# Kernel optimization log

Measured on AMD Instinct MI355X. Metric: run time of the kernel, lower is better.

Reference implementation:

```python
import jax, jax.numpy as jnp
import numpy as np

WS = 8            # window size (square)
NUM_HEADS = 8
DIM = 256
IMG = 256         # feature map H=W for mask construction
SHIFT = WS // 2
B = 4


def _rel_pos_index(Wh, Ww):
    coords = np.stack(np.meshgrid(np.arange(Wh), np.arange(Ww), indexing='ij'))  # (2,Wh,Ww)
    cf = coords.reshape(2, -1)
    rel = cf[:, :, None] - cf[:, None, :]        # (2,N,N)
    rel = rel.transpose(1, 2, 0).astype(np.int64)
    rel[..., 0] += Wh - 1
    rel[..., 1] += Ww - 1
    rel[..., 0] *= 2 * Ww - 1
    return rel.sum(-1)                           # (N,N)


def _shift_mask(H, W, ws, ss):
    # standard Swin shifted-window attention mask: (nW, ws*ws, ws*ws) with 0 / -100
    img = np.zeros((H, W), dtype=np.float32)
    cnt = 0
    for hs in (slice(0, -ws), slice(-ws, -ss), slice(-ss, None)):
        for wsl in (slice(0, -ws), slice(-ws, -ss), slice(-ss, None)):
            img[hs, wsl] = cnt
            cnt += 1
    m = img.reshape(H // ws, ws, W // ws, ws).transpose(0, 2, 1, 3).reshape(-1, ws * ws)
    am = m[:, None, :] - m[:, :, None]
    return np.where(am != 0, np.float32(-100.0), np.float32(0.0))


def setup_inputs() -> dict:
    key = jax.random.key(0)
    ks = jax.random.split(key, 10)
    nW = (IMG // WS) ** 2
    B_ = B * nW
    N = WS * WS
    x = jax.random.normal(ks[0], (B_, N, DIM), dtype=jnp.float32)
    y = jax.random.normal(ks[1], (B_, N, DIM), dtype=jnp.float32)
    mask = jnp.asarray(_shift_mask(IMG, IMG, WS, SHIFT))
    s = 0.02
    q_w = jax.random.normal(ks[2], (DIM, DIM), dtype=jnp.float32) * s
    q_b = jnp.zeros((DIM,), dtype=jnp.float32)
    kv_w = jax.random.normal(ks[3], (2 * DIM, DIM), dtype=jnp.float32) * s
    kv_b = jnp.zeros((2 * DIM,), dtype=jnp.float32)
    proj_w = jax.random.normal(ks[4], (DIM, DIM), dtype=jnp.float32) * s
    proj_b = jnp.zeros((DIM,), dtype=jnp.float32)
    rpb_table = jax.random.normal(ks[5], ((2 * WS - 1) ** 2, NUM_HEADS), dtype=jnp.float32) * s
    return {"x": x, "y": y, "mask": mask, "q_w": q_w, "q_b": q_b,
            "kv_w": kv_w, "kv_b": kv_b, "proj_w": proj_w, "proj_b": proj_b,
            "rpb_table": rpb_table}


def reference(x, y, mask, q_w, q_b, kv_w, kv_b, proj_w, proj_b, rpb_table):
    B_, N, C = x.shape
    H = NUM_HEADS
    hd = C // H
    scale = hd ** -0.5
    # projections
    q = (x @ q_w.T + q_b).reshape(B_, N, H, hd).transpose(0, 2, 1, 3) * scale  # (B_,H,N,hd)
    kv = (y @ kv_w.T + kv_b).reshape(B_, N, 2, H, hd)
    k = kv[:, :, 0].transpose(0, 2, 1, 3)  # (B_,H,N,hd)
    v = kv[:, :, 1].transpose(0, 2, 1, 3)
    attn = jnp.einsum('bhid,bhjd->bhij', q, k)  # (B_,H,N,N)
    # relative position bias gathered from table
    rpi = jnp.asarray(_rel_pos_index(WS, WS))           # (N,N) int
    bias = rpb_table[rpi.reshape(-1)].reshape(N, N, H).transpose(2, 0, 1)  # (H,N,N)
    attn = attn + bias[None]
    # shifted-window mask
    nW = mask.shape[0]
    attn = attn.reshape(B_ // nW, nW, H, N, N) + mask[None, :, None]
    attn = attn.reshape(B_, H, N, N)
    attn = jax.nn.softmax(attn, axis=-1)
    out = jnp.einsum('bhij,bhjd->bhid', attn, v)        # (B_,H,N,hd)
    out = out.transpose(0, 2, 1, 3).reshape(B_, N, C)
    return out @ proj_w.T + proj_b
```

## Files before the change

kernel.cpp:

```cpp
#include <hip/hip_runtime.h>

typedef _Float16 half_t;
typedef _Float16 half8  __attribute__((ext_vector_type(8)));
typedef _Float16 half4v __attribute__((ext_vector_type(4)));
typedef float    f32x4  __attribute__((ext_vector_type(4)));

#define ROWB   528
#define S_A    0
#define S_B    33792
#define SMEM_BYTES 67584
#define SCALE  0.17677669529663687f

__global__ __launch_bounds__(256) void swin_prep(
    const float* __restrict__ q_w, const float* __restrict__ kv_w,
    const float* __restrict__ proj_w, const float* __restrict__ rpb,
    const float* __restrict__ mask,
    half_t* __restrict__ w16, half_t* __restrict__ fused)
{
    int t = blockIdx.x * 256 + threadIdx.x;
    if (t < 65536)        w16[t] = (half_t)(q_w[t] * SCALE);
    else if (t < 196608)  w16[t] = (half_t)kv_w[t - 65536];
    else if (t < 262144)  w16[t] = (half_t)proj_w[t - 196608];
    else if (t < 393216) {
        int u = t - 262144;
        int cls = u >> 15, rest = u & 32767;
        int h = rest >> 12, i = (rest >> 6) & 63, j = rest & 63;
        int idx = ((i >> 3) - (j >> 3) + 7) * 15 + ((i & 7) - (j & 7) + 7);
        int wsel = (cls == 0) ? 0 : (cls == 1) ? 31 : (cls == 2) ? 992 : 1023;
        fused[u] = (half_t)(rpb[idx * 8 + h] + mask[(size_t)wsel * 4096 + i * 64 + j]);
    }
}

static __device__ __forceinline__ unsigned pk2(float a, float b) {
    union { _Float16 h[2]; unsigned u; } t;
    t.h[0] = (_Float16)a; t.h[1] = (_Float16)b; return t.u;
}

#define BUILD_FRAG(dst, P0, P1)                                          \
    do {                                                                 \
        union { unsigned u[4]; half8 h; } _u;                            \
        _Pragma("unroll")                                                \
        for (int p = 0; p < 4; ++p) {                                    \
            int _src = (p >> 1) ? srcB : srcA;                           \
            unsigned _rlo = (unsigned)__shfl((int)(P0)[p & 1], _src);    \
            unsigned _rhi = (unsigned)__shfl((int)(P1)[p & 1], _src);    \
            _u.u[p] = hi ? _rhi : _rlo;                                  \
        }                                                                \
        dst = _u.h;                                                      \
    } while (0)

__global__ __launch_bounds__(512, 2) void swin_main(
    const float* __restrict__ x, const float* __restrict__ y,
    const float* __restrict__ q_b, const float* __restrict__ kv_b,
    const float* __restrict__ proj_b,
    const half_t* __restrict__ w16, const half_t* __restrict__ fused,
    float* __restrict__ out)
{
    __shared__ __align__(16) char sm[SMEM_BYTES];
    const int tid  = threadIdx.x;
    const int w    = tid >> 6;
    const int lane = tid & 63;
    const int l15  = lane & 15;
    const int g    = lane >> 4;
    const int b    = blockIdx.x;
    const int jf0  = w * 32;
    const int srcA = ((2 * g) & 3) * 16 + l15;
    const int srcB = ((2 * g + 1) & 3) * 16 + l15;
    const int hi   = g >> 1;

    const float* xb = x + (size_t)b * 16384;
    const float* yb = y + (size_t)b * 16384;
    const half_t* wkv = w16 + 65536;

    {
        float4 fx[8], fy[8];
        #pragma unroll
        for (int it = 0; it < 4; ++it) {
            int c = tid + it * 512;
            int row = c >> 5, c8 = c & 31;
            fx[it*2+0] = *(const float4*)(xb + row * 256 + c8 * 8);
            fx[it*2+1] = *(const float4*)(xb + row * 256 + c8 * 8 + 4);
            fy[it*2+0] = *(const float4*)(yb + row * 256 + c8 * 8);
            fy[it*2+1] = *(const float4*)(yb + row * 256 + c8 * 8 + 4);
        }
        #pragma unroll
        for (int it = 0; it < 4; ++it) {
            int c = tid + it * 512;
            int row = c >> 5, c8 = c & 31;
            half8 hx, hy;
            #pragma unroll
            for (int e = 0; e < 4; ++e) {
                hx[e]   = (half_t)(&fx[it*2+0].x)[e];
                hx[e+4] = (half_t)(&fx[it*2+1].x)[e];
                hy[e]   = (half_t)(&fy[it*2+0].x)[e];
                hy[e+4] = (half_t)(&fy[it*2+1].x)[e];
            }
            int off = row * ROWB + c8 * 16;
            *(half8*)(sm + S_A + off) = hx;
            *(half8*)(sm + S_B + off) = hy;
        }
    }
    __syncthreads();

    f32x4 kacc[2][4], vacc[4][2];
    #pragma unroll
    for (int ft = 0; ft < 2; ++ft)
        #pragma unroll
        for (int tok = 0; tok < 4; ++tok) {
            f32x4 z = {0.f,0.f,0.f,0.f}; kacc[ft][tok] = z; vacc[tok][ft] = z;
        }
    #pragma unroll
    for (int kh = 0; kh < 4; ++kh) {
        half8 wbk[2][2], wbv[2][2];
        #pragma unroll
        for (int k2 = 0; k2 < 2; ++k2) {
            int k0 = (kh * 2 + k2) * 32 + g * 8;
            #pragma unroll
            for (int ft = 0; ft < 2; ++ft) {
                int jf = jf0 + ft * 16 + l15;
                wbk[k2][ft] = *(const half8*)(wkv + jf * 256 + k0);
                wbv[k2][ft] = *(const half8*)(wkv + (256 + jf) * 256 + k0);
            }
        }
        #pragma unroll
        for (int k2 = 0; k2 < 2; ++k2) {
            int k0 = (kh * 2 + k2) * 32 + g * 8;
            half8 a[4];
            #pragma unroll
            for (int tok = 0; tok < 4; ++tok)
                a[tok] = *(const half8*)(sm + S_B + (tok * 16 + l15) * ROWB + k0 * 2);
            #pragma unroll
            for (int ft = 0; ft < 2; ++ft)
                #pragma unroll
                for (int tok = 0; tok < 4; ++tok) {
                    kacc[ft][tok] = __builtin_amdgcn_mfma_f32_16x16x32_f16(wbk[k2][ft], a[tok], kacc[ft][tok], 0, 0, 0);
                    vacc[tok][ft] = __builtin_amdgcn_mfma_f32_16x16x32_f16(a[tok], wbv[k2][ft], vacc[tok][ft], 0, 0, 0);
                }
        }
    }

    unsigned kp[2][4][2], vp[4][2][2];
    #pragma unroll
    for (int ft = 0; ft < 2; ++ft) {
        float4 kb4 = *(const float4*)(kv_b + jf0 + ft * 16 + g * 4);
        #pragma unroll
        for (int tok = 0; tok < 4; ++tok) {
            kp[ft][tok][0] = pk2(kacc[ft][tok][0] + kb4.x, kacc[ft][tok][1] + kb4.y);
            kp[ft][tok][1] = pk2(kacc[ft][tok][2] + kb4.z, kacc[ft][tok][3] + kb4.w);
        }
    }
    #pragma unroll
    for (int ft = 0; ft < 2; ++ft) {
        float vb = kv_b[256 + jf0 + ft * 16 + l15];
        #pragma unroll
        for (int tok = 0; tok < 4; ++tok) {
            vp[tok][ft][0] = pk2(vacc[tok][ft][0] + vb, vacc[tok][ft][1] + vb);
            vp[tok][ft][1] = pk2(vacc[tok][ft][2] + vb, vacc[tok][ft][3] + vb);
        }
    }

    unsigned qp[2][4][2];
    {
        f32x4 qacc[2][4];
        #pragma unroll
        for (int ft = 0; ft < 2; ++ft)
            #pragma unroll
            for (int tok = 0; tok < 4; ++tok) { f32x4 z = {0.f,0.f,0.f,0.f}; qacc[ft][tok] = z; }
        #pragma unroll
        for (int kh = 0; kh < 4; ++kh) {
            half8 wbq[2][2];
            #pragma unroll
            for (int k2 = 0; k2 < 2; ++k2) {
                int k0 = (kh * 2 + k2) * 32 + g * 8;
                #pragma unroll
                for (int ft = 0; ft < 2; ++ft)
                    wbq[k2][ft] = *(const half8*)(w16 + (jf0 + ft * 16 + l15) * 256 + k0);
            }
            #pragma unroll
            for (int k2 = 0; k2 < 2; ++k2) {
                int k0 = (kh * 2 + k2) * 32 + g * 8;
                half8 a[4];
                #pragma unroll
                for (int tok = 0; tok < 4; ++tok)
                    a[tok] = *(const half8*)(sm + S_A + (tok * 16 + l15) * ROWB + k0 * 2);
                #pragma unroll
                for (int ft = 0; ft < 2; ++ft)
                    #pragma unroll
                    for (int tok = 0; tok < 4; ++tok)
                        qacc[ft][tok] = __builtin_amdgcn_mfma_f32_16x16x32_f16(wbq[k2][ft], a[tok], qacc[ft][tok], 0, 0, 0);
            }
        }
        #pragma unroll
        for (int ft = 0; ft < 2; ++ft) {
            float4 qb4 = *(const float4*)(q_b + jf0 + ft * 16 + g * 4);
            #pragma unroll
            for (int tok = 0; tok < 4; ++tok) {
                qp[ft][tok][0] = pk2(qacc[ft][tok][0] + qb4.x * SCALE, qacc[ft][tok][1] + qb4.y * SCALE);
                qp[ft][tok][1] = pk2(qacc[ft][tok][2] + qb4.z * SCALE, qacc[ft][tok][3] + qb4.w * SCALE);
            }
        }
    }

    f32x4 o[2][4];
    {
        half8 ka[4], qf[4];
        #pragma unroll
        for (int mt = 0; mt < 4; ++mt) BUILD_FRAG(ka[mt], kp[0][mt], kp[1][mt]);
        #pragma unroll
        for (int nt = 0; nt < 4; ++nt) BUILD_FRAG(qf[nt], qp[0][nt], qp[1][nt]);

        f32x4 t[4][4];
        #pragma unroll
        for (int mt = 0; mt < 4; ++mt)
            #pragma unroll
            for (int nt = 0; nt < 4; ++nt) {
                f32x4 z = {0.f,0.f,0.f,0.f};
                t[mt][nt] = __builtin_amdgcn_mfma_f32_16x16x32_f16(ka[mt], qf[nt], z, 0, 0, 0);
            }

        const int wi = b & 1023;
        const int cls = ((((wi >> 5) == 31) ? 2 : 0)) | (((wi & 31) == 31) ? 1 : 0);
        const half_t* fb = fused + ((size_t)cls * 8 + w) * 4096;
        half4v fm[4][4];
        #pragma unroll
        for (int nt = 0; nt < 4; ++nt)
            #pragma unroll
            for (int mt = 0; mt < 4; ++mt)
                fm[nt][mt] = *(const half4v*)(fb + (nt * 16 + l15) * 64 + mt * 16 + g * 4);

        #pragma unroll
        for (int nt = 0; nt < 4; ++nt) {
            #pragma unroll
            for (int mt = 0; mt < 4; ++mt)
                #pragma unroll
                for (int r = 0; r < 4; ++r)
                    t[mt][nt][r] += (float)fm[nt][mt][r];
            float m = -1e30f;
            #pragma unroll
            for (int mt = 0; mt < 4; ++mt)
                #pragma unroll
                for (int r = 0; r < 4; ++r) m = fmaxf(m, t[mt][nt][r]);
            m = fmaxf(m, __shfl_xor(m, 16));
            m = fmaxf(m, __shfl_xor(m, 32));
            float s = 0.f;
            #pragma unroll
            for (int mt = 0; mt < 4; ++mt)
                #pragma unroll
                for (int r = 0; r < 4; ++r) {
                    float p = __expf(t[mt][nt][r] - m);
                    t[mt][nt][r] = p;
                    s += p;
                }
            s += __shfl_xor(s, 16);
            s += __shfl_xor(s, 32);
            float inv = 1.f / s;
            #pragma unroll
            for (int mt = 0; mt < 4; ++mt)
                #pragma unroll
                for (int r = 0; r < 4; ++r) t[mt][nt][r] *= inv;
        }

        unsigned pp[4][4][2];
        #pragma unroll
        for (int mt = 0; mt < 4; ++mt)
            #pragma unroll
            for (int nt = 0; nt < 4; ++nt) {
                pp[mt][nt][0] = pk2(t[mt][nt][0], t[mt][nt][1]);
                pp[mt][nt][1] = pk2(t[mt][nt][2], t[mt][nt][3]);
            }

        #pragma unroll
        for (int dt = 0; dt < 2; ++dt)
            #pragma unroll
            for (int nt = 0; nt < 4; ++nt) { f32x4 z = {0.f,0.f,0.f,0.f}; o[dt][nt] = z; }
        #pragma unroll
        for (int kc = 0; kc < 2; ++kc) {
            half8 va[2], pf[4];
            #pragma unroll
            for (int dt = 0; dt < 2; ++dt) BUILD_FRAG(va[dt], vp[kc*2+0][dt], vp[kc*2+1][dt]);
            #pragma unroll
            for (int nt = 0; nt < 4; ++nt) BUILD_FRAG(pf[nt], pp[kc*2+0][nt], pp[kc*2+1][nt]);
            #pragma unroll
            for (int dt = 0; dt < 2; ++dt)
                #pragma unroll
                for (int nt = 0; nt < 4; ++nt)
                    o[dt][nt] = __builtin_amdgcn_mfma_f32_16x16x32_f16(va[dt], pf[nt], o[dt][nt], 0, 0, 0);
        }
    }

    __syncthreads();

    #pragma unroll
    for (int nt = 0; nt < 4; ++nt) {
        int i = nt * 16 + l15;
        #pragma unroll
        for (int dt = 0; dt < 2; ++dt) {
            half4v ov;
            ov[0] = (half_t)o[dt][nt][0];
            ov[1] = (half_t)o[dt][nt][1];
            ov[2] = (half_t)o[dt][nt][2];
            ov[3] = (half_t)o[dt][nt][3];
            *(half4v*)(sm + S_B + i * ROWB + (jf0 + dt * 16 + g * 4) * 2) = ov;
        }
    }
    __syncthreads();

    {
        const half_t* wp = w16 + 196608;
        f32x4 dacc[4][2];
        #pragma unroll
        for (int mt = 0; mt < 4; ++mt)
            #pragma unroll
            for (int ft = 0; ft < 2; ++ft) { f32x4 z = {0.f,0.f,0.f,0.f}; dacc[mt][ft] = z; }
        #pragma unroll
        for (int kh = 0; kh < 4; ++kh) {
            half8 wbp[2][2];
            #pragma unroll
            for (int k2 = 0; k2 < 2; ++k2) {
                int k0 = (kh * 2 + k2) * 32 + g * 8;
                #pragma unroll
                for (int ft = 0; ft < 2; ++ft)
                    wbp[k2][ft] = *(const half8*)(wp + (jf0 + ft * 16 + l15) * 256 + k0);
            }
            #pragma unroll
            for (int k2 = 0; k2 < 2; ++k2) {
                int k0 = (kh * 2 + k2) * 32 + g * 8;
                half8 a[4];
                #pragma unroll
                for (int mt = 0; mt < 4; ++mt)
                    a[mt] = *(const half8*)(sm + S_B + (mt * 16 + l15) * ROWB + k0 * 2);
                #pragma unroll
                for (int mt = 0; mt < 4; ++mt)
                    #pragma unroll
                    for (int ft = 0; ft < 2; ++ft)
                        dacc[mt][ft] = __builtin_amdgcn_mfma_f32_16x16x32_f16(wbp[k2][ft], a[mt], dacc[mt][ft], 0, 0, 0);
            }
        }
        float* ob = out + (size_t)b * 16384;
        #pragma unroll
        for (int ft = 0; ft < 2; ++ft) {
            float4 pb4 = *(const float4*)(proj_b + jf0 + ft * 16 + g * 4);
            #pragma unroll
            for (int mt = 0; mt < 4; ++mt) {
                float4 v;
                v.x = dacc[mt][ft][0] + pb4.x;
                v.y = dacc[mt][ft][1] + pb4.y;
                v.z = dacc[mt][ft][2] + pb4.z;
                v.w = dacc[mt][ft][3] + pb4.w;
                *(float4*)(ob + (mt * 16 + l15) * 256 + jf0 + ft * 16 + g * 4) = v;
            }
        }
    }
}

extern "C" void kernel_launch(void* const* d_in, const int* in_sizes, int n_in,
                              void* d_out, int out_size, void* d_ws, size_t ws_size,
                              hipStream_t stream) {
    const float* x      = (const float*)d_in[0];
    const float* y      = (const float*)d_in[1];
    const float* mask   = (const float*)d_in[2];
    const float* q_w    = (const float*)d_in[3];
    const float* q_b    = (const float*)d_in[4];
    const float* kv_w   = (const float*)d_in[5];
    const float* kv_b   = (const float*)d_in[6];
    const float* proj_w = (const float*)d_in[7];
    const float* proj_b = (const float*)d_in[8];
    const float* rpb    = (const float*)d_in[9];

    half_t* w16   = (half_t*)d_ws;
    half_t* fused = (half_t*)((char*)d_ws + 524288);

    swin_prep<<<1536, 256, 0, stream>>>(q_w, kv_w, proj_w, rpb, mask, w16, fused);
    swin_main<<<4096, 512, 0, stream>>>(x, y, q_b, kv_b, proj_b,
                                        w16, fused, (float*)d_out);
}
```

Measured before the change: 469.4 us.

## Make main kernel persistent over 8 windows per block with setprio and nontemporal stores

Each block now loops over 8 windows instead of one, and the grid shrinks from 4096 to 512 blocks. Bias vectors are hoisted out of the loop, MFMA sections are wrapped in s_setprio, and output stores become nontemporal. Barriers are replaced with a custom lgkmcnt wait plus s_barrier so the next window's global loads can be issued before the barrier. The goal is to amortize block launch and bias loads. The risk is fewer blocks (512 over 256 CUs at 2 per CU) with less latency hiding, plus a serial tail.

```diff
diff --git a/kernel.cpp b/kernel.cpp
--- a/kernel.cpp
+++ b/kernel.cpp
@@ -10,6 +10,13 @@
 #define S_B    33792
 #define SMEM_BYTES 67584
 #define SCALE  0.17677669529663687f
+#define NWPB   8
+
+#define BAR() do { \
+    asm volatile("s_waitcnt lgkmcnt(0)" ::: "memory"); \
+    __builtin_amdgcn_s_barrier(); \
+    __builtin_amdgcn_sched_barrier(0); \
+} while (0)
 
 __global__ __launch_bounds__(256) void swin_prep(
     const float* __restrict__ q_w, const float* __restrict__ kv_w,
@@ -62,17 +69,31 @@
     const int lane = tid & 63;
     const int l15  = lane & 15;
     const int g    = lane >> 4;
-    const int b    = blockIdx.x;
     const int jf0  = w * 32;
     const int srcA = ((2 * g) & 3) * 16 + l15;
     const int srcB = ((2 * g + 1) & 3) * 16 + l15;
     const int hi   = g >> 1;
-
-    const float* xb = x + (size_t)b * 16384;
-    const float* yb = y + (size_t)b * 16384;
     const half_t* wkv = w16 + 65536;
-
-    {
+    const half_t* wpj = w16 + 196608;
+
+    float4 kb4[2], qb4s[2], pb4[2];
+    float  vb[2];
+    #pragma unroll
+    for (int ft = 0; ft < 2; ++ft) {
+        kb4[ft]  = *(const float4*)(kv_b + jf0 + ft * 16 + g * 4);
+        float4 q4 = *(const float4*)(q_b + jf0 + ft * 16 + g * 4);
+        qb4s[ft].x = q4.x * SCALE; qb4s[ft].y = q4.y * SCALE;
+        qb4s[ft].z = q4.z * SCALE; qb4s[ft].w = q4.w * SCALE;
+        pb4[ft]  = *(const float4*)(proj_b + jf0 + ft * 16 + g * 4);
+        vb[ft]   = kv_b[256 + jf0 + ft * 16 + l15];
+    }
+
+    #pragma unroll 1
+    for (int wd = 0; wd < NWPB; ++wd) {
+        const int b = blockIdx.x * NWPB + wd;
+        const float* xb = x + (size_t)b * 16384;
+        const float* yb = y + (size_t)b * 16384;
+
         float4 fx[8], fy[8];
         #pragma unroll
         for (int it = 0; it < 4; ++it) {
@@ -83,6 +104,9 @@
             fy[it*2+0] = *(const float4*)(yb + row * 256 + c8 * 8);
             fy[it*2+1] = *(const float4*)(yb + row * 256 + c8 * 8 + 4);
         }
+
+        BAR();
+
         #pragma unroll
         for (int it = 0; it < 4; ++it) {
             int c = tid + it * 512;
@@ -99,82 +123,28 @@
             *(half8*)(sm + S_A + off) = hx;
             *(half8*)(sm + S_B + off) = hy;
         }
-    }
-    __syncthreads();
-
-    f32x4 kacc[2][4], vacc[4][2];
-    #pragma unroll
-    for (int ft = 0; ft < 2; ++ft)
-        #pragma unroll
-        for (int tok = 0; tok < 4; ++tok) {
-            f32x4 z = {0.f,0.f,0.f,0.f}; kacc[ft][tok] = z; vacc[tok][ft] = z;
-        }
-    #pragma unroll
-    for (int kh = 0; kh < 4; ++kh) {
-        half8 wbk[2][2], wbv[2][2];
-        #pragma unroll
-        for (int k2 = 0; k2 < 2; ++k2) {
-            int k0 = (kh * 2 + k2) * 32 + g * 8;
-            #pragma unroll
-            for (int ft = 0; ft < 2; ++ft) {
-                int jf = jf0 + ft * 16 + l15;
-                wbk[k2][ft] = *(const half8*)(wkv + jf * 256 + k0);
-                wbv[k2][ft] = *(const half8*)(wkv + (256 + jf) * 256 + k0);
-            }
-        }
-        #pragma unroll
-        for (int k2 = 0; k2 < 2; ++k2) {
-            int k0 = (kh * 2 + k2) * 32 + g * 8;
-            half8 a[4];
-            #pragma unroll
-            for (int tok = 0; tok < 4; ++tok)
-                a[tok] = *(const half8*)(sm + S_B + (tok * 16 + l15) * ROWB + k0 * 2);
-            #pragma unroll
-            for (int ft = 0; ft < 2; ++ft)
-                #pragma unroll
-                for (int tok = 0; tok < 4; ++tok) {
-                    kacc[ft][tok] = __builtin_amdgcn_mfma_f32_16x16x32_f16(wbk[k2][ft], a[tok], kacc[ft][tok], 0, 0, 0);
-                    vacc[tok][ft] = __builtin_amdgcn_mfma_f32_16x16x32_f16(a[tok], wbv[k2][ft], vacc[tok][ft], 0, 0, 0);
-                }
-        }
-    }
-
-    unsigned kp[2][4][2], vp[4][2][2];
-    #pragma unroll
-    for (int ft = 0; ft < 2; ++ft) {
-        float4 kb4 = *(const float4*)(kv_b + jf0 + ft * 16 + g * 4);
-        #pragma unroll
-        for (int tok = 0; tok < 4; ++tok) {
-            kp[ft][tok][0] = pk2(kacc[ft][tok][0] + kb4.x, kacc[ft][tok][1] + kb4.y);
-            kp[ft][tok][1] = pk2(kacc[ft][tok][2] + kb4.z, kacc[ft][tok][3] + kb4.w);
-        }
-    }
-    #pragma unroll
-    for (int ft = 0; ft < 2; ++ft) {
-        float vb = kv_b[256 + jf0 + ft * 16 + l15];
-        #pragma unroll
-        for (int tok = 0; tok < 4; ++tok) {
-            vp[tok][ft][0] = pk2(vacc[tok][ft][0] + vb, vacc[tok][ft][1] + vb);
-            vp[tok][ft][1] = pk2(vacc[tok][ft][2] + vb, vacc[tok][ft][3] + vb);
-        }
-    }
-
-    unsigned qp[2][4][2];
-    {
-        f32x4 qacc[2][4];
+
+        BAR();
+
+        f32x4 kacc[2][4], vacc[4][2];
         #pragma unroll
         for (int ft = 0; ft < 2; ++ft)
             #pragma unroll
-            for (int tok = 0; tok < 4; ++tok) { f32x4 z = {0.f,0.f,0.f,0.f}; qacc[ft][tok] = z; }
+            for (int tok = 0; tok < 4; ++tok) {
+                f32x4 z = {0.f,0.f,0.f,0.f}; kacc[ft][tok] = z; vacc[tok][ft] = z;
+            }
         #pragma unroll
         for (int kh = 0; kh < 4; ++kh) {
-            half8 wbq[2][2];
+            half8 wbk[2][2], wbv[2][2];
             #pragma unroll
             for (int k2 = 0; k2 < 2; ++k2) {
                 int k0 = (kh * 2 + k2) * 32 + g * 8;
                 #pragma unroll
-                for (int ft = 0; ft < 2; ++ft)
-                    wbq[k2][ft] = *(const half8*)(w16 + (jf0 + ft * 16 + l15) * 256 + k0);
+                for (int ft = 0; ft < 2; ++ft) {
+                    int jf = jf0 + ft * 16 + l15;
+                    wbk[k2][ft] = *(const half8*)(wkv + jf * 256 + k0);
+                    wbv[k2][ft] = *(const half8*)(wkv + (256 + jf) * 256 + k0);
+                }
             }
             #pragma unroll
             for (int k2 = 0; k2 < 2; ++k2) {
@@ -182,172 +152,225 @@
                 half8 a[4];
                 #pragma unroll
                 for (int tok = 0; tok < 4; ++tok)
-                    a[tok] = *(const half8*)(sm + S_A + (tok * 16 + l15) * ROWB + k0 * 2);
+                    a[tok] = *(const half8*)(sm + S_B + (tok * 16 + l15) * ROWB + k0 * 2);
+                __builtin_amdgcn_s_setprio(1);
                 #pragma unroll
                 for (int ft = 0; ft < 2; ++ft)
                     #pragma unroll
+                    for (int tok = 0; tok < 4; ++tok) {
+                        kacc[ft][tok] = __builtin_amdgcn_mfma_f32_16x16x32_f16(wbk[k2][ft], a[tok], kacc[ft][tok], 0, 0, 0);
+                        vacc[tok][ft] = __builtin_amdgcn_mfma_f32_16x16x32_f16(a[tok], wbv[k2][ft], vacc[tok][ft], 0, 0, 0);
+                    }
+                __builtin_amdgcn_s_setprio(0);
+            }
+        }
+
+        unsigned kp[2][4][2], vp[4][2][2];
+        #pragma unroll
+        for (int ft = 0; ft < 2; ++ft)
+            #pragma unroll
+            for (int tok = 0; tok < 4; ++tok) {
+                kp[ft][tok][0] = pk2(kacc[ft][tok][0] + kb4[ft].x, kacc[ft][tok][1] + kb4[ft].y);
+                kp[ft][tok][1] = pk2(kacc[ft][tok][2] + kb4[ft].z, kacc[ft][tok][3] + kb4[ft].w);
+                vp[tok][ft][0] = pk2(vacc[tok][ft][0] + vb[ft], vacc[tok][ft][1] + vb[ft]);
+                vp[tok][ft][1] = pk2(vacc[tok][ft][2] + vb[ft], vacc[tok][ft][3] + vb[ft]);
+            }
+
+        unsigned qp[2][4][2];
+        {
+            f32x4 qacc[2][4];
+            #pragma unroll
+            for (int ft = 0; ft < 2; ++ft)
+                #pragma unroll
+                for (int tok = 0; tok < 4; ++tok) { f32x4 z = {0.f,0.f,0.f,0.f}; qacc[ft][tok] = z; }
+            #pragma unroll
+            for (int kh = 0; kh < 4; ++kh) {
+                half8 wbq[2][2];
+                #pragma unroll
+                for (int k2 = 0; k2 < 2; ++k2) {
+                    int k0 = (kh * 2 + k2) * 32 + g * 8;
+                    #pragma unroll
+                    for (int ft = 0; ft < 2; ++ft)
+                        wbq[k2][ft] = *(const half8*)(w16 + (jf0 + ft * 16 + l15) * 256 + k0);
+                }
+                #pragma unroll
+                for (int k2 = 0; k2 < 2; ++k2) {
+                    int k0 = (kh * 2 + k2) * 32 + g * 8;
+                    half8 a[4];
+                    #pragma unroll
                     for (int tok = 0; tok < 4; ++tok)
-                        qacc[ft][tok] = __builtin_amdgcn_mfma_f32_16x16x32_f16(wbq[k2][ft], a[tok], qacc[ft][tok], 0, 0, 0);
-            }
-        }
-        #pragma unroll
-        for (int ft = 0; ft < 2; ++ft) {
-            float4 qb4 = *(const float4*)(q_b + jf0 + ft * 16 + g * 4);
-            #pragma unroll
-            for (int tok = 0; tok < 4; ++tok) {
-                qp[ft][tok][0] = pk2(qacc[ft][tok][0] + qb4.x * SCALE, qacc[ft][tok][1] + qb4.y * SCALE);
-                qp[ft][tok][1] = pk2(qacc[ft][tok][2] + qb4.z * SCALE, qacc[ft][tok][3] + qb4.w * SCALE);
-            }
-        }
-    }
-
-    f32x4 o[2][4];
-    {
-        half8 ka[4], qf[4];
-        #pragma unroll
-        for (int mt = 0; mt < 4; ++mt) BUILD_FRAG(ka[mt], kp[0][mt], kp[1][mt]);
-        #pragma unroll
-        for (int nt = 0; nt < 4; ++nt) BUILD_FRAG(qf[nt], qp[0][nt], qp[1][nt]);
-
-        f32x4 t[4][4];
-        #pragma unroll
-        for (int mt = 0; mt < 4; ++mt)
+                        a[tok] = *(const half8*)(sm + S_A + (tok * 16 + l15) * ROWB + k0 * 2);
+                    __builtin_amdgcn_s_setprio(1);
+                    #pragma unroll
+                    for (int ft = 0; ft < 2; ++ft)
+                        #pragma unroll
+                        for (int tok = 0; tok < 4; ++tok)
+                            qacc[ft][tok] = __builtin_amdgcn_mfma_f32_16x16x32_f16(wbq[k2][ft], a[tok], qacc[ft][tok], 0, 0, 0);
+                    __builtin_amdgcn_s_setprio(0);
+                }
+            }
+            #pragma unroll
+            for (int ft = 0; ft < 2; ++ft)
+                #pragma unroll
+                for (int tok = 0; tok < 4; ++tok) {
+                    qp[ft][tok][0] = pk2(qacc[ft][tok][0] + qb4s[ft].x, qacc[ft][tok][1] + qb4s[ft].y);
+                    qp[ft][tok][1] = pk2(qacc[ft][tok][2] + qb4s[ft].z, qacc[ft][tok][3] + qb4s[ft].w);
+                }
+        }
+
+        f32x4 o[2][4];
+        {
+            half8 ka[4], qf[4];
+            #pragma unroll
+            for (int mt = 0; mt < 4; ++mt) BUILD_FRAG(ka[mt], kp[0][mt], kp[1][mt]);
+            #pragma unroll
+            for (int nt = 0; nt < 4; ++nt) BUILD_FRAG(qf[nt], qp[0][nt], qp[1][nt]);
+
+            f32x4 t[4][4];
+            __builtin_amdgcn_s_setprio(1);
+            #pragma unroll
+            for (int mt = 0; mt < 4; ++mt)
+                #pragma unroll
+                for (int nt = 0; nt < 4; ++nt) {
+                    f32x4 z = {0.f,0.f,0.f,0.f};
+                    t[mt][nt] = __builtin_amdgcn_mfma_f32_16x16x32_f16(ka[mt], qf[nt], z, 0, 0, 0);
+                }
+            __builtin_amdgcn_s_setprio(0);
+
+            const int wi = b & 1023;
+            const int cls = ((((wi >> 5) == 31) ? 2 : 0)) | (((wi & 31) == 31) ? 1 : 0);
+            const half_t* fb = fused + ((size_t)cls * 8 + w) * 4096;
+            half4v fm[4][4];
+            #pragma unroll
+            for (int nt = 0; nt < 4; ++nt)
+                #pragma unroll
+                for (int mt = 0; mt < 4; ++mt)
+                    fm[nt][mt] = *(const half4v*)(fb + (nt * 16 + l15) * 64 + mt * 16 + g * 4);
+
             #pragma unroll
             for (int nt = 0; nt < 4; ++nt) {
-                f32x4 z = {0.f,0.f,0.f,0.f};
-                t[mt][nt] = __builtin_amdgcn_mfma_f32_16x16x32_f16(ka[mt], qf[nt], z, 0, 0, 0);
-            }
-
-        const int wi = b & 1023;
-        const int cls = ((((wi >> 5) == 31) ? 2 : 0)) | (((wi & 31) == 31) ? 1 : 0);
-        const half_t* fb = fused + ((size_t)cls * 8 + w) * 4096;
-        half4v fm[4][4];
-        #pragma unroll
-        for (int nt = 0; nt < 4; ++nt)
+                #pragma unroll
+                for (int mt = 0; mt < 4; ++mt)
+                    #pragma unroll
+                    for (int r = 0; r < 4; ++r)
+                        t[mt][nt][r] += (float)fm[nt][mt][r];
+                float m = -1e30f;
+                #pragma unroll
+                for (int mt = 0; mt < 4; ++mt)
+                    #pragma unroll
+                    for (int r = 0; r < 4; ++r) m = fmaxf(m, t[mt][nt][r]);
+                m = fmaxf(m, __shfl_xor(m, 16));
+                m = fmaxf(m, __shfl_xor(m, 32));
+                float s = 0.f;
+                #pragma unroll
+                for (int mt = 0; mt < 4; ++mt)
+                    #pragma unroll
+                    for (int r = 0; r < 4; ++r) {
+                        float p = __expf(t[mt][nt][r] - m);
+                        t[mt][nt][r] = p;
+                        s += p;
+                    }
+                s += __shfl_xor(s, 16);
+                s += __shfl_xor(s, 32);
+                float inv = 1.f / s;
+                #pragma unroll
+                for (int mt = 0; mt < 4; ++mt)
+                    #pragma unroll
+                    for (int r = 0; r < 4; ++r) t[mt][nt][r] *= inv;
+            }
+
+            unsigned pp[4][4][2];
             #pragma unroll
             for (int mt = 0; mt < 4; ++mt)
-                fm[nt][mt] = *(const half4v*)(fb + (nt * 16 + l15) * 64 + mt * 16 + g * 4);
+                #pragma unroll
+                for (int nt = 0; nt < 4; ++nt) {
+                    pp[mt][nt][0] = pk2(t[mt][nt][0], t[mt][nt][1]);
+                    pp[mt][nt][1] = pk2(t[mt][nt][2], t[mt][nt][3]);
+                }
+
+            #pragma unroll
+            for (int dt = 0; dt < 2; ++dt)
+                #pragma unroll
+                for (int nt = 0; nt < 4; ++nt) { f32x4 z = {0.f,0.f,0.f,0.f}; o[dt][nt] = z; }
+            #pragma unroll
+            for (int kc = 0; kc < 2; ++kc) {
+                half8 va[2], pf[4];
+                #pragma unroll
+                for (int dt = 0; dt < 2; ++dt) BUILD_FRAG(va[dt], vp[kc*2+0][dt], vp[kc*2+1][dt]);
+                #pragma unroll
+                for (int nt = 0; nt < 4; ++nt) BUILD_FRAG(pf[nt], pp[kc*2+0][nt], pp[kc*2+1][nt]);
+                __builtin_amdgcn_s_setprio(1);
+                #pragma unroll
+                for (int dt = 0; dt < 2; ++dt)
+                    #pragma unroll
+                    for (int nt = 0; nt < 4; ++nt)
+                        o[dt][nt] = __builtin_amdgcn_mfma_f32_16x16x32_f16(va[dt], pf[nt], o[dt][nt], 0, 0, 0);
+                __builtin_amdgcn_s_setprio(0);
+            }
+        }
+
+        BAR();
 
         #pragma unroll
         for (int nt = 0; nt < 4; ++nt) {
+            int i = nt * 16 + l15;
+            #pragma unroll
+            for (int dt = 0; dt < 2; ++dt) {
+                half4v ov;
+                ov[0] = (half_t)o[dt][nt][0];
+                ov[1] = (half_t)o[dt][nt][1];
+                ov[2] = (half_t)o[dt][nt][2];
+                ov[3] = (half_t)o[dt][nt][3];
+                *(half4v*)(sm + S_B + i * ROWB + (jf0 + dt * 16 + g * 4) * 2) = ov;
+            }
+        }
+
+        BAR();
+
+        {
+            f32x4 dacc[4][2];
             #pragma unroll
             for (int mt = 0; mt < 4; ++mt)
                 #pragma unroll
-                for (int r = 0; r < 4; ++r)
-                    t[mt][nt][r] += (float)fm[nt][mt][r];
-            float m = -1e30f;
-            #pragma unroll
-            for (int mt = 0; mt < 4; ++mt)
-                #pragma unroll
-                for (int r = 0; r < 4; ++r) m = fmaxf(m, t[mt][nt][r]);
-            m = fmaxf(m, __shfl_xor(m, 16));
-            m = fmaxf(m, __shfl_xor(m, 32));
-            float s = 0.f;
-            #pragma unroll
-            for (int mt = 0; mt < 4; ++mt)
-                #pragma unroll
-                for (int r = 0; r < 4; ++r) {
-                    float p = __expf(t[mt][nt][r] - m);
-                    t[mt][nt][r] = p;
-                    s += p;
-                }
-            s += __shfl_xor(s, 16);
-            s += __shfl_xor(s, 32);
-            float inv = 1.f / s;
-            #pragma unroll
-            for (int mt = 0; mt < 4; ++mt)
-                #pragma unroll
-                for (int r = 0; r < 4; ++r) t[mt][nt][r] *= inv;
-        }
-
-        unsigned pp[4][4][2];
-        #pragma unroll
-        for (int mt = 0; mt < 4; ++mt)
-            #pragma unroll
-            for (int nt = 0; nt < 4; ++nt) {
-                pp[mt][nt][0] = pk2(t[mt][nt][0], t[mt][nt][1]);
-                pp[mt][nt][1] = pk2(t[mt][nt][2], t[mt][nt][3]);
-            }
-
-        #pragma unroll
-        for (int dt = 0; dt < 2; ++dt)
-            #pragma unroll
-            for (int nt = 0; nt < 4; ++nt) { f32x4 z = {0.f,0.f,0.f,0.f}; o[dt][nt] = z; }
-        #pragma unroll
-        for (int kc = 0; kc < 2; ++kc) {
-            half8 va[2], pf[4];
-            #pragma unroll
-            for (int dt = 0; dt < 2; ++dt) BUILD_FRAG(va[dt], vp[kc*2+0][dt], vp[kc*2+1][dt]);
-            #pragma unroll
-            for (int nt = 0; nt < 4; ++nt) BUILD_FRAG(pf[nt], pp[kc*2+0][nt], pp[kc*2+1][nt]);
-            #pragma unroll
-            for (int dt = 0; dt < 2; ++dt)
-                #pragma unroll
-                for (int nt = 0; nt < 4; ++nt)
-                    o[dt][nt] = __builtin_amdgcn_mfma_f32_16x16x32_f16(va[dt], pf[nt], o[dt][nt], 0, 0, 0);
-        }
-    }
-
-    __syncthreads();
-
-    #pragma unroll
-    for (int nt = 0; nt < 4; ++nt) {
-        int i = nt * 16 + l15;
-        #pragma unroll
-        for (int dt = 0; dt < 2; ++dt) {
-            half4v ov;
-            ov[0] = (half_t)o[dt][nt][0];
-            ov[1] = (half_t)o[dt][nt][1];
-            ov[2] = (half_t)o[dt][nt][2];
-            ov[3] = (half_t)o[dt][nt][3];
-            *(half4v*)(sm + S_B + i * ROWB + (jf0 + dt * 16 + g * 4) * 2) = ov;
-        }
-    }
-    __syncthreads();
-
-    {
-        const half_t* wp = w16 + 196608;
-        f32x4 dacc[4][2];
-        #pragma unroll
-        for (int mt = 0; mt < 4; ++mt)
-            #pragma unroll
-            for (int ft = 0; ft < 2; ++ft) { f32x4 z = {0.f,0.f,0.f,0.f}; dacc[mt][ft] = z; }
-        #pragma unroll
-        for (int kh = 0; kh < 4; ++kh) {
-            half8 wbp[2][2];
-            #pragma unroll
-            for (int k2 = 0; k2 < 2; ++k2) {
-                int k0 = (kh * 2 + k2) * 32 + g * 8;
-                #pragma unroll
-                for (int ft = 0; ft < 2; ++ft)
-                    wbp[k2][ft] = *(const half8*)(wp + (jf0 + ft * 16 + l15) * 256 + k0);
-            }
-            #pragma unroll
-            for (int k2 = 0; k2 < 2; ++k2) {
-                int k0 = (kh * 2 + k2) * 32 + g * 8;
-                half8 a[4];
-                #pragma unroll
-                for (int mt = 0; mt < 4; ++mt)
-                    a[mt] = *(const half8*)(sm + S_B + (mt * 16 + l15) * ROWB + k0 * 2);
-                #pragma unroll
-                for (int mt = 0; mt < 4; ++mt)
+                for (int ft = 0; ft < 2; ++ft) { f32x4 z = {0.f,0.f,0.f,0.f}; dacc[mt][ft] = z; }
+            #pragma unroll
+            for (int kh = 0; kh < 4; ++kh) {
+                half8 wbp[2][2];
+                #pragma unroll
+                for (int k2 = 0; k2 < 2; ++k2) {
+                    int k0 = (kh * 2 + k2) * 32 + g * 8;
                     #pragma unroll
                     for (int ft = 0; ft < 2; ++ft)
-                        dacc[mt][ft] = __builtin_amdgcn_mfma_f32_16x16x32_f16(wbp[k2][ft], a[mt], dacc[mt][ft], 0, 0, 0);
-            }
-        }
-        float* ob = out + (size_t)b * 16384;
-        #pragma unroll
-        for (int ft = 0; ft < 2; ++ft) {
-            float4 pb4 = *(const float4*)(proj_b + jf0 + ft * 16 + g * 4);
-            #pragma unroll
-            for (int mt = 0; mt < 4; ++mt) {
-                float4 v;
-                v.x = dacc[mt][ft][0] + pb4.x;
-                v.y = dacc[mt][ft][1] + pb4.y;
-                v.z = dacc[mt][ft][2] + pb4.z;
-                v.w = dacc[mt][ft][3] + pb4.w;
-                *(float4*)(ob + (mt * 16 + l15) * 256 + jf0 + ft * 16 + g * 4) = v;
+                        wbp[k2][ft] = *(const half8*)(wpj + (jf0 + ft * 16 + l15) * 256 + k0);
+                }
+                #pragma unroll
+                for (int k2 = 0; k2 < 2; ++k2) {
+                    int k0 = (kh * 2 + k2) * 32 + g * 8;
+                    half8 a[4];
+                    #pragma unroll
+                    for (int mt = 0; mt < 4; ++mt)
+                        a[mt] = *(const half8*)(sm + S_B + (mt * 16 + l15) * ROWB + k0 * 2);
+                    __builtin_amdgcn_s_setprio(1);
+                    #pragma unroll
+                    for (int mt = 0; mt < 4; ++mt)
+                        #pragma unroll
+                        for (int ft = 0; ft < 2; ++ft)
+                            dacc[mt][ft] = __builtin_amdgcn_mfma_f32_16x16x32_f16(wbp[k2][ft], a[mt], dacc[mt][ft], 0, 0, 0);
+                    __builtin_amdgcn_s_setprio(0);
+                }
+            }
+            float* ob = out + (size_t)b * 16384;
+            #pragma unroll
+            for (int ft = 0; ft < 2; ++ft) {
+                #pragma unroll
+                for (int mt = 0; mt < 4; ++mt) {
+                    f32x4 v;
+                    v[0] = dacc[mt][ft][0] + pb4[ft].x;
+                    v[1] = dacc[mt][ft][1] + pb4[ft].y;
+                    v[2] = dacc[mt][ft][2] + pb4[ft].z;
+                    v[3] = dacc[mt][ft][3] + pb4[ft].w;
+                    __builtin_nontemporal_store(v, (f32x4*)(ob + (mt * 16 + l15) * 256 + jf0 + ft * 16 + g * 4));
+                }
             }
         }
     }
@@ -361,8 +384,8 @@
     const float* mask   = (const float*)d_in[2];
     const float* q_w    = (const float*)d_in[3];
     const float* q_b    = (const float*)d_in[4];
+    const float* kv_b   = (const float*)d_in[6];
     const float* kv_w   = (const float*)d_in[5];
-    const float* kv_b   = (const float*)d_in[6];
     const float* proj_w = (const float*)d_in[7];
     const float* proj_b = (const float*)d_in[8];
     const float* rpb    = (const float*)d_in[9];
@@ -371,6 +394,6 @@
     half_t* fused = (half_t*)((char*)d_ws + 524288);
 
     swin_prep<<<1536, 256, 0, stream>>>(q_w, kv_w, proj_w, rpb, mask, w16, fused);
-    swin_main<<<4096, 512, 0, stream>>>(x, y, q_b, kv_b, proj_b,
-                                        w16, fused, (float*)d_out);
+    swin_main<<<512, 512, 0, stream>>>(x, y, q_b, kv_b, proj_b,
+                                       w16, fused, (float*)d_out);
 }
```

Measured after the change: 486.1 us. 3.6% more time.

## Split fused Swin window attention into QKV, attention and projection kernels

Applied to the files above, without the earlier changes.

Breaks the single fused kernel into three kernels (QKV projection, attention, output projection) that exchange Q, K, transposed V and O through global workspace in fp16, chunked by available workspace size. The aim is to remove register pressure and cross-lane shuffles in the fused kernel and allow different occupancy per stage. In exchange it adds a large global-memory round trip per window and extra kernel launches.

```diff
diff --git a/kernel.cpp b/kernel.cpp
--- a/kernel.cpp
+++ b/kernel.cpp
@@ -8,7 +8,8 @@
 #define ROWB   528
 #define S_A    0
 #define S_B    33792
-#define SMEM_BYTES 67584
+#define K1_SMEM 67584
+#define K3_SMEM 33792
 #define SCALE  0.17677669529663687f
 
 __global__ __launch_bounds__(256) void swin_prep(
@@ -35,6 +36,9 @@
     union { _Float16 h[2]; unsigned u; } t;
     t.h[0] = (_Float16)a; t.h[1] = (_Float16)b; return t.u;
 }
+static __device__ __forceinline__ half4v h4(float a, float b, float c, float d) {
+    half4v v; v[0] = (half_t)a; v[1] = (half_t)b; v[2] = (half_t)c; v[3] = (half_t)d; return v;
+}
 
 #define BUILD_FRAG(dst, P0, P1)                                          \
     do {                                                                 \
@@ -49,28 +53,26 @@
         dst = _u.h;                                                      \
     } while (0)
 
-__global__ __launch_bounds__(512, 2) void swin_main(
+__global__ __launch_bounds__(512, 1) void swin_qkv(
     const float* __restrict__ x, const float* __restrict__ y,
     const float* __restrict__ q_b, const float* __restrict__ kv_b,
-    const float* __restrict__ proj_b,
-    const half_t* __restrict__ w16, const half_t* __restrict__ fused,
-    float* __restrict__ out)
+    const half_t* __restrict__ w16,
+    half_t* __restrict__ Qg, half_t* __restrict__ Kg, half_t* __restrict__ Vtg,
+    int b0)
 {
-    __shared__ __align__(16) char sm[SMEM_BYTES];
+    __shared__ __align__(16) char sm[K1_SMEM];
     const int tid  = threadIdx.x;
     const int w    = tid >> 6;
     const int lane = tid & 63;
     const int l15  = lane & 15;
     const int g    = lane >> 4;
-    const int b    = blockIdx.x;
+    const int bl   = blockIdx.x;
+    const int b    = b0 + bl;
     const int jf0  = w * 32;
-    const int srcA = ((2 * g) & 3) * 16 + l15;
-    const int srcB = ((2 * g + 1) & 3) * 16 + l15;
-    const int hi   = g >> 1;
+    const half_t* wkv = w16 + 65536;
 
     const float* xb = x + (size_t)b * 16384;
     const float* yb = y + (size_t)b * 16384;
-    const half_t* wkv = w16 + 65536;
 
     {
         float4 fx[8], fy[8];
@@ -138,28 +140,29 @@
                 }
         }
     }
-
-    unsigned kp[2][4][2], vp[4][2][2];
-    #pragma unroll
-    for (int ft = 0; ft < 2; ++ft) {
-        float4 kb4 = *(const float4*)(kv_b + jf0 + ft * 16 + g * 4);
-        #pragma unroll
-        for (int tok = 0; tok < 4; ++tok) {
-            kp[ft][tok][0] = pk2(kacc[ft][tok][0] + kb4.x, kacc[ft][tok][1] + kb4.y);
-            kp[ft][tok][1] = pk2(kacc[ft][tok][2] + kb4.z, kacc[ft][tok][3] + kb4.w);
-        }
-    }
-    #pragma unroll
-    for (int ft = 0; ft < 2; ++ft) {
-        float vb = kv_b[256 + jf0 + ft * 16 + l15];
-        #pragma unroll
-        for (int tok = 0; tok < 4; ++tok) {
-            vp[tok][ft][0] = pk2(vacc[tok][ft][0] + vb, vacc[tok][ft][1] + vb);
-            vp[tok][ft][1] = pk2(vacc[tok][ft][2] + vb, vacc[tok][ft][3] + vb);
-        }
-    }
-
-    unsigned qp[2][4][2];
+    {
+        half_t* Kw = Kg + (size_t)bl * 16384;
+        #pragma unroll
+        for (int ft = 0; ft < 2; ++ft) {
+            float4 kb4 = *(const float4*)(kv_b + jf0 + ft * 16 + g * 4);
+            #pragma unroll
+            for (int tok = 0; tok < 4; ++tok)
+                *(half4v*)(Kw + (tok * 16 + l15) * 256 + jf0 + ft * 16 + g * 4) =
+                    h4(kacc[ft][tok][0] + kb4.x, kacc[ft][tok][1] + kb4.y,
+                       kacc[ft][tok][2] + kb4.z, kacc[ft][tok][3] + kb4.w);
+        }
+        half_t* Vw = Vtg + (size_t)bl * 16384;
+        #pragma unroll
+        for (int ft = 0; ft < 2; ++ft) {
+            float vb = kv_b[256 + jf0 + ft * 16 + l15];
+            #pragma unroll
+            for (int tok = 0; tok < 4; ++tok)
+                *(half4v*)(Vw + (jf0 + ft * 16 + l15) * 64 + tok * 16 + g * 4) =
+                    h4(vacc[tok][ft][0] + vb, vacc[tok][ft][1] + vb,
+                       vacc[tok][ft][2] + vb, vacc[tok][ft][3] + vb);
+    }
+    }
+
     {
         f32x4 qacc[2][4];
         #pragma unroll
@@ -190,165 +193,202 @@
                         qacc[ft][tok] = __builtin_amdgcn_mfma_f32_16x16x32_f16(wbq[k2][ft], a[tok], qacc[ft][tok], 0, 0, 0);
             }
         }
+        half_t* Qw = Qg + (size_t)bl * 16384;
         #pragma unroll
         for (int ft = 0; ft < 2; ++ft) {
-            float4 qb4 = *(const float4*)(q_b + jf0 + ft * 16 + g * 4);
-            #pragma unroll
-            for (int tok = 0; tok < 4; ++tok) {
-                qp[ft][tok][0] = pk2(qacc[ft][tok][0] + qb4.x * SCALE, qacc[ft][tok][1] + qb4.y * SCALE);
-                qp[ft][tok][1] = pk2(qacc[ft][tok][2] + qb4.z * SCALE, qacc[ft][tok][3] + qb4.w * SCALE);
+            float4 q4 = *(const float4*)(q_b + jf0 + ft * 16 + g * 4);
+            #pragma unroll
+            for (int tok = 0; tok < 4; ++tok)
+                *(half4v*)(Qw + (tok * 16 + l15) * 256 + jf0 + ft * 16 + g * 4) =
+                    h4(qacc[ft][tok][0] + q4.x * SCALE, qacc[ft][tok][1] + q4.y * SCALE,
+                       qacc[ft][tok][2] + q4.z * SCALE, qacc[ft][tok][3] + q4.w * SCALE);
+        }
+    }
+}
+
+__global__ __launch_bounds__(512, 1) void swin_attn(
+    const half_t* __restrict__ Qg, const half_t* __restrict__ Kg,
+    const half_t* __restrict__ Vtg, const half_t* __restrict__ fused,
+    half_t* __restrict__ Og, int b0)
+{
+    const int tid  = threadIdx.x;
+    const int w    = tid >> 6;
+    const int lane = tid & 63;
+    const int l15  = lane & 15;
+    const int g    = lane >> 4;
+    const int bl   = blockIdx.x;
+    const int b    = b0 + bl;
+    const int jf0  = w * 32;
+    const int srcA = ((2 * g) & 3) * 16 + l15;
+    const int srcB = ((2 * g + 1) & 3) * 16 + l15;
+    const int hi   = g >> 1;
+
+    const half_t* Qw = Qg + (size_t)bl * 16384;
+    const half_t* Kw = Kg + (size_t)bl * 16384;
+    const half_t* Vw = Vtg + (size_t)bl * 16384;
+
+    half8 ka[4], qf[4];
+    #pragma unroll
+    for (int mt = 0; mt < 4; ++mt)
+        ka[mt] = *(const half8*)(Kw + (mt * 16 + l15) * 256 + jf0 + g * 8);
+    #pragma unroll
+    for (int nt = 0; nt < 4; ++nt)
+        qf[nt] = *(const half8*)(Qw + (nt * 16 + l15) * 256 + jf0 + g * 8);
+
+    f32x4 t[4][4];
+    #pragma unroll
+    for (int mt = 0; mt < 4; ++mt)
+        #pragma unroll
+        for (int nt = 0; nt < 4; ++nt) {
+            f32x4 z = {0.f,0.f,0.f,0.f};
+            t[mt][nt] = __builtin_amdgcn_mfma_f32_16x16x32_f16(ka[mt], qf[nt], z, 0, 0, 0);
+        }
+
+    const int wi = b & 1023;
+    const int cls = ((((wi >> 5) == 31) ? 2 : 0)) | (((wi & 31) == 31) ? 1 : 0);
+    const half_t* fb = fused + ((size_t)cls * 8 + w) * 4096;
+    half4v fm[4][4];
+    #pragma unroll
+    for (int nt = 0; nt < 4; ++nt)
+        #pragma unroll
+        for (int mt = 0; mt < 4; ++mt)
+            fm[nt][mt] = *(const half4v*)(fb + (nt * 16 + l15) * 64 + mt * 16 + g * 4);
+
+    #pragma unroll
+    for (int nt = 0; nt < 4; ++nt) {
+        #pragma unroll
+        for (int mt = 0; mt < 4; ++mt)
+            #pragma unroll
+            for (int r = 0; r < 4; ++r)
+                t[mt][nt][r] += (float)fm[nt][mt][r];
+        float m = -1e30f;
+        #pragma unroll
+        for (int mt = 0; mt < 4; ++mt)
+            #pragma unroll
+            for (int r = 0; r < 4; ++r) m = fmaxf(m, t[mt][nt][r]);
+        m = fmaxf(m, __shfl_xor(m, 16));
+        m = fmaxf(m, __shfl_xor(m, 32));
+        float s = 0.f;
+        #pragma unroll
+        for (int mt = 0; mt < 4; ++mt)
+            #pragma unroll
+            for (int r = 0; r < 4; ++r) {
+                float p = __expf(t[mt][nt][r] - m);
+                t[mt][nt][r] = p;
+                s += p;
             }
-        }
-    }
+        s += __shfl_xor(s, 16);
+        s += __shfl_xor(s, 32);
+        float inv = 1.f / s;
+        #pragma unroll
+        for (int mt = 0; mt < 4; ++mt)
+            #pragma unroll
+            for (int r = 0; r < 4; ++r) t[mt][nt][r] *= inv;
+    }
+
+    unsigned pp[4][4][2];
+    #pragma unroll
+    for (int mt = 0; mt < 4; ++mt)
+        #pragma unroll
+        for (int nt = 0; nt < 4; ++nt) {
+            pp[mt][nt][0] = pk2(t[mt][nt][0], t[mt][nt][1]);
+            pp[mt][nt][1] = pk2(t[mt][nt][2], t[mt][nt][3]);
+        }
 
     f32x4 o[2][4];
-    {
-        half8 ka[4], qf[4];
-        #pragma unroll
-        for (int mt = 0; mt < 4; ++mt) BUILD_FRAG(ka[mt], kp[0][mt], kp[1][mt]);
-        #pragma unroll
-        for (int nt = 0; nt < 4; ++nt) BUILD_FRAG(qf[nt], qp[0][nt], qp[1][nt]);
-
-        f32x4 t[4][4];
-        #pragma unroll
-        for (int mt = 0; mt < 4; ++mt)
-            #pragma unroll
-            for (int nt = 0; nt < 4; ++nt) {
-                f32x4 z = {0.f,0.f,0.f,0.f};
-                t[mt][nt] = __builtin_amdgcn_mfma_f32_16x16x32_f16(ka[mt], qf[nt], z, 0, 0, 0);
-            }
-
-        const int wi = b & 1023;
-        const int cls = ((((wi >> 5) == 31) ? 2 : 0)) | (((wi & 31) == 31) ? 1 : 0);
-        const half_t* fb = fused + ((size_t)cls * 8 + w) * 4096;
-        half4v fm[4][4];
-        #pragma unroll
-        for (int nt = 0; nt < 4; ++nt)
+    #pragma unroll
+    for (int dt = 0; dt < 2; ++dt)
+        #pragma unroll
+        for (int nt = 0; nt < 4; ++nt) { f32x4 z = {0.f,0.f,0.f,0.f}; o[dt][nt] = z; }
+    #pragma unroll
+    for (int kc = 0; kc < 2; ++kc) {
+        half8 va[2], pf[4];
+        #pragma unroll
+        for (int dt = 0; dt < 2; ++dt)
+            va[dt] = *(const half8*)(Vw + (jf0 + dt * 16 + l15) * 64 + kc * 32 + g * 8);
+        #pragma unroll
+        for (int nt = 0; nt < 4; ++nt) BUILD_FRAG(pf[nt], pp[kc*2+0][nt], pp[kc*2+1][nt]);
+        #pragma unroll
+        for (int dt = 0; dt < 2; ++dt)
+            #pragma unroll
+            for (int nt = 0; nt < 4; ++nt)
+                o[dt][nt] = __builtin_amdgcn_mfma_f32_16x16x32_f16(va[dt], pf[nt], o[dt][nt], 0, 0, 0);
+    }
+
+    half_t* Ow = Og + (size_t)bl * 16384;
+    #pragma unroll
+    for (int nt = 0; nt < 4; ++nt)
+        #pragma unroll
+        for (int dt = 0; dt < 2; ++dt)
+            *(half4v*)(Ow + (nt * 16 + l15) * 256 + jf0 + dt * 16 + g * 4) =
+                h4(o[dt][nt][0], o[dt][nt][1], o[dt][nt][2], o[dt][nt][3]);
+}
+
+__global__ __launch_bounds__(512, 2) void swin_proj(
+    const half_t* __restrict__ Og, const float* __restrict__ proj_b,
+    const half_t* __restrict__ w16, float* __restrict__ out, int b0)
+{
+    __shared__ __align__(16) char sm[K3_SMEM];
+    const int tid  = threadIdx.x;
+    const int w    = tid >> 6;
+    const int lane = tid & 63;
+    const int l15  = lane & 15;
+    const int g    = lane >> 4;
+    const int bl   = blockIdx.x;
+    const int b    = b0 + bl;
+    const int jf0  = w * 32;
+    const half_t* wpj = w16 + 196608;
+    const half_t* Ow = Og + (size_t)bl * 16384;
+
+    #pragma unroll
+    for (int it = 0; it < 4; ++it) {
+        int c = tid + it * 512;
+        int row = c >> 5, c8 = c & 31;
+        *(half8*)(sm + row * ROWB + c8 * 16) = *(const half8*)(Ow + row * 256 + c8 * 8);
+    }
+    __syncthreads();
+
+    f32x4 dacc[4][2];
+    #pragma unroll
+    for (int mt = 0; mt < 4; ++mt)
+        #pragma unroll
+        for (int ft = 0; ft < 2; ++ft) { f32x4 z = {0.f,0.f,0.f,0.f}; dacc[mt][ft] = z; }
+    #pragma unroll
+    for (int kh = 0; kh < 4; ++kh) {
+        half8 wbp[2][2];
+        #pragma unroll
+        for (int k2 = 0; k2 < 2; ++k2) {
+            int k0 = (kh * 2 + k2) * 32 + g * 8;
+            #pragma unroll
+            for (int ft = 0; ft < 2; ++ft)
+                wbp[k2][ft] = *(const half8*)(wpj + (jf0 + ft * 16 + l15) * 256 + k0);
+        }
+        #pragma unroll
+        for (int k2 = 0; k2 < 2; ++k2) {
+            int k0 = (kh * 2 + k2) * 32 + g * 8;
+            half8 a[4];
             #pragma unroll
             for (int mt = 0; mt < 4; ++mt)
-                fm[nt][mt] = *(const half4v*)(fb + (nt * 16 + l15) * 64 + mt * 16 + g * 4);
-
-        #pragma unroll
-        for (int nt = 0; nt < 4; ++nt) {
+                a[mt] = *(const half8*)(sm + (mt * 16 + l15) * ROWB + k0 * 2);
             #pragma unroll
             for (int mt = 0; mt < 4; ++mt)
                 #pragma unroll
-                for (int r = 0; r < 4; ++r)
-                    t[mt][nt][r] += (float)fm[nt][mt][r];
-            float m = -1e30f;
-            #pragma unroll
-            for (int mt = 0; mt < 4; ++mt)
-                #pragma unroll
-                for (int r = 0; r < 4; ++r) m = fmaxf(m, t[mt][nt][r]);
-            m = fmaxf(m, __shfl_xor(m, 16));
-            m = fmaxf(m, __shfl_xor(m, 32));
-            float s = 0.f;
-            #pragma unroll
-            for (int mt = 0; mt < 4; ++mt)
-                #pragma unroll
-                for (int r = 0; r < 4; ++r) {
-                    float p = __expf(t[mt][nt][r] - m);
-                    t[mt][nt][r] = p;
-                    s += p;
-                }
-            s += __shfl_xor(s, 16);
-            s += __shfl_xor(s, 32);
-            float inv = 1.f / s;
-            #pragma unroll
-            for (int mt = 0; mt < 4; ++mt)
-                #pragma unroll
-                for (int r = 0; r < 4; ++r) t[mt][nt][r] *= inv;
-        }
-
-        unsigned pp[4][4][2];
-        #pragma unroll
-        for (int mt = 0; mt < 4; ++mt)
-            #pragma unroll
-            for (int nt = 0; nt < 4; ++nt) {
-                pp[mt][nt][0] = pk2(t[mt][nt][0], t[mt][nt][1]);
-                pp[mt][nt][1] = pk2(t[mt][nt][2], t[mt][nt][3]);
-            }
-
-        #pragma unroll
-        for (int dt = 0; dt < 2; ++dt)
-            #pragma unroll
-            for (int nt = 0; nt < 4; ++nt) { f32x4 z = {0.f,0.f,0.f,0.f}; o[dt][nt] = z; }
-        #pragma unroll
-        for (int kc = 0; kc < 2; ++kc) {
-            half8 va[2], pf[4];
-            #pragma unroll
-            for (int dt = 0; dt < 2; ++dt) BUILD_FRAG(va[dt], vp[kc*2+0][dt], vp[kc*2+1][dt]);
-            #pragma unroll
-            for (int nt = 0; nt < 4; ++nt) BUILD_FRAG(pf[nt], pp[kc*2+0][nt], pp[kc*2+1][nt]);
-            #pragma unroll
-            for (int dt = 0; dt < 2; ++dt)
-                #pragma unroll
-                for (int nt = 0; nt < 4; ++nt)
-                    o[dt][nt] = __builtin_amdgcn_mfma_f32_16x16x32_f16(va[dt], pf[nt], o[dt][nt], 0, 0, 0);
-        }
-    }
-
-    __syncthreads();
-
-    #pragma unroll
-    for (int nt = 0; nt < 4; ++nt) {
-        int i = nt * 16 + l15;
-        #pragma unroll
-        for (int dt = 0; dt < 2; ++dt) {
-            half4v ov;
-            ov[0] = (half_t)o[dt][nt][0];
-            ov[1] = (half_t)o[dt][nt][1];
-            ov[2] = (half_t)o[dt][nt][2];
-            ov[3] = (half_t)o[dt][nt][3];
-            *(half4v*)(sm + S_B + i * ROWB + (jf0 + dt * 16 + g * 4) * 2) = ov;
-        }
-    }
-    __syncthreads();
-
-    {
-        const half_t* wp = w16 + 196608;
-        f32x4 dacc[4][2];
-        #pragma unroll
-        for (int mt = 0; mt < 4; ++mt)
-            #pragma unroll
-            for (int ft = 0; ft < 2; ++ft) { f32x4 z = {0.f,0.f,0.f,0.f}; dacc[mt][ft] = z; }
-        #pragma unroll
-        for (int kh = 0; kh < 4; ++kh) {
-            half8 wbp[2][2];
-            #pragma unroll
-            for (int k2 = 0; k2 < 2; ++k2) {
-                int k0 = (kh * 2 + k2) * 32 + g * 8;
-                #pragma unroll
                 for (int ft = 0; ft < 2; ++ft)
-                    wbp[k2][ft] = *(const half8*)(wp + (jf0 + ft * 16 + l15) * 256 + k0);
-            }
-            #pragma unroll
-            for (int k2 = 0; k2 < 2; ++k2) {
-                int k0 = (kh * 2 + k2) * 32 + g * 8;
-                half8 a[4];
-                #pragma unroll
-                for (int mt = 0; mt < 4; ++mt)
-                    a[mt] = *(const half8*)(sm + S_B + (mt * 16 + l15) * ROWB + k0 * 2);
-                #pragma unroll
-                for (int mt = 0; mt < 4; ++mt)
-                    #pragma unroll
-                    for (int ft = 0; ft < 2; ++ft)
-                        dacc[mt][ft] = __builtin_amdgcn_mfma_f32_16x16x32_f16(wbp[k2][ft], a[mt], dacc[mt][ft], 0, 0, 0);
-            }
-        }
-        float* ob = out + (size_t)b * 16384;
-        #pragma unroll
-        for (int ft = 0; ft < 2; ++ft) {
-            float4 pb4 = *(const float4*)(proj_b + jf0 + ft * 16 + g * 4);
-            #pragma unroll
-            for (int mt = 0; mt < 4; ++mt) {
-                float4 v;
-                v.x = dacc[mt][ft][0] + pb4.x;
-                v.y = dacc[mt][ft][1] + pb4.y;
-                v.z = dacc[mt][ft][2] + pb4.z;
-                v.w = dacc[mt][ft][3] + pb4.w;
-                *(float4*)(ob + (mt * 16 + l15) * 256 + jf0 + ft * 16 + g * 4) = v;
-            }
+                    dacc[mt][ft] = __builtin_amdgcn_mfma_f32_16x16x32_f16(wbp[k2][ft], a[mt], dacc[mt][ft], 0, 0, 0);
+        }
+    }
+    float* ob = out + (size_t)b * 16384;
+    #pragma unroll
+    for (int ft = 0; ft < 2; ++ft) {
+        float4 pb4 = *(const float4*)(proj_b + jf0 + ft * 16 + g * 4);
+        #pragma unroll
+        for (int mt = 0; mt < 4; ++mt) {
+            f32x4 v;
+            v[0] = dacc[mt][ft][0] + pb4.x;
+            v[1] = dacc[mt][ft][1] + pb4.y;
+            v[2] = dacc[mt][ft][2] + pb4.z;
+            v[3] = dacc[mt][ft][3] + pb4.w;
+            *(f32x4*)(ob + (mt * 16 + l15) * 256 + jf0 + ft * 16 + g * 4) = v;
         }
     }
 }
@@ -366,11 +406,29 @@
     const float* proj_w = (const float*)d_in[7];
     const float* proj_b = (const float*)d_in[8];
     const float* rpb    = (const float*)d_in[9];
+    float* out          = (float*)d_out;
 
     half_t* w16   = (half_t*)d_ws;
     half_t* fused = (half_t*)((char*)d_ws + 524288);
+    const size_t base = 786432;
+
+    int nchunk = 1;
+    while (nchunk < 64) {
+        size_t per = (size_t)(4096 / nchunk) * 16384 * 2;
+        if (base + 4 * per <= ws_size) break;
+        nchunk *= 2;
+    }
+    const int W = 4096 / nchunk;
+    half_t* Qg  = (half_t*)((char*)d_ws + base);
+    half_t* Kg  = Qg  + (size_t)W * 16384;
+    half_t* Vtg = Kg  + (size_t)W * 16384;
+    half_t* Og  = Vtg + (size_t)W * 16384;
 
     swin_prep<<<1536, 256, 0, stream>>>(q_w, kv_w, proj_w, rpb, mask, w16, fused);
-    swin_main<<<4096, 512, 0, stream>>>(x, y, q_b, kv_b, proj_b,
-                                        w16, fused, (float*)d_out);
-}
+    for (int c = 0; c < nchunk; ++c) {
+        int b0 = c * W;
+        swin_qkv<<<W, 512, 0, stream>>>(x, y, q_b, kv_b, w16, Qg, Kg, Vtg, b0);
+        swin_attn<<<W, 512, 0, stream>>>(Qg, Kg, Vtg, fused, Og, b0);
+        swin_proj<<<W, 512, 0, stream>>>(Og, proj_b, w16, out, b0);
+    }
+}
```

Measured after the change: 635.6 us. 1.35x slower.
